# Kernel tuning notes

Measured on AMD Instinct MI355X. Metric: run time of the kernel, lower is better.

The kernel has to match this reference:

```python
import jax, jax.numpy as jnp
import numpy as np

B, N, P, E = 64, 512, 256, 4096          # batch, nodes (stations), partition nodes, edges
NUM_NWP, LP, F = 8, 16, 32               # num_nwp, local_points, local_cnn_dims
NT, ED, H, W = 8, 8, 64, 8               # num_temp, edge_feature_dims, decf_mlp_hidden, weight_function_dim
G, RH = 64, 256                          # gnn_dim, readout_hid_dim
H1, Q = 128, 9                           # mlp_hid_dim1, num quantiles


def setup_inputs() -> dict:
    key = jax.random.key(0)
    ks = iter(jax.random.split(key, 40))
    def rn(shape, s=0.05):
        return jax.random.normal(next(ks), shape, dtype=jnp.float32) * s
    # one-hot incidence matrices: each edge has one left (partition) node and one right node
    lidx = jax.random.randint(next(ks), (E,), 0, P)
    ridx = jax.random.randint(next(ks), (E,), 0, N)
    linc = jnp.zeros((P, E), jnp.float32).at[lidx, jnp.arange(E)].set(1.0)
    rinc = jnp.zeros((E, N), jnp.float32).at[jnp.arange(E), ridx].set(1.0)
    inp = {
        "x1": jax.random.normal(next(ks), (B, NUM_NWP * N, LP), dtype=jnp.float32),
        "x2": jax.random.normal(next(ks), (B, NT), dtype=jnp.float32),
        # LocalConv1D grouped conv (torch OIW layout: [Cout, Cin/groups, K])
        "conv_w": rn((F * N, NUM_NWP, LP)), "conv_b": rn((F * N,)),
        # WDSGCN2 edge-weight MLP
        "k1_w": rn((H, ED)), "k1_b": rn((H,)),
        "k2_w": rn((H, NT)),
        "k3_w": rn((H, F)),
        "k4_w": rn((H, F)),
        "k5_w": rn((W, H)), "k5_b": rn((W,)),
        "gc_w": rn((G, F * W)), "gc_b": rn((G,)),
        # readout
        "r0_w": rn((RH, G * P)),
        "r1_w": rn((RH, NT)), "r1_b": rn((RH,)),
        "r2_w": rn((RH, P)),
        "r3_w": rn((P, RH)), "r3_b": rn((P,)),
        # SMlp (forward uses l1 -> ELU -> l3 only)
        "l1_w": rn((H1, NT + G)), "l1_b": rn((H1,)),
        "l3_w": rn((Q, H1)), "l3_b": rn((Q,)),
        # buffers
        "ef": jax.random.normal(next(ks), (E, ED + 1), dtype=jnp.float32),
        "linc": linc,
        "rinc": rinc,
        "cap_feature": jax.random.normal(next(ks), (P,), dtype=jnp.float32),
        "partition_idx": jnp.arange(P, dtype=jnp.int32) * (N // P),
    }
    return inp


def reference(x1, x2, conv_w, conv_b, k1_w, k1_b, k2_w, k3_w, k4_w, k5_w, k5_b,
              gc_w, gc_b, r0_w, r1_w, r1_b, r2_w, r3_w, r3_b,
              l1_w, l1_b, l3_w, l3_b, ef, linc, rinc, cap_feature, partition_idx):
    b = x1.shape[0]
    # --- LocalConv1D: grouped conv1d (valid padding, output length 1) + ReLU ---
    y = jax.lax.conv_general_dilated(x1, conv_w, (1,), 'VALID',
                                     dimension_numbers=('NCH', 'OIH', 'NCH'),
                                     feature_group_count=N)
    x = jax.nn.relu(y + conv_b[None, :, None]).reshape(b, N, F)      # [B,N,F]
    # --- WDSGCN2: per-edge weight kernel ---
    kern = ef[:, :-1] @ k1_w.T + k1_b                                # [E,H]
    kern = kern[None] + (x2 @ k2_w.T)[:, None, :]                    # [B,E,H]
    xp = x[:, partition_idx, :]                                      # [B,P,F]
    kern = kern + jnp.einsum('pe,bpf->bef', linc, xp) @ k3_w.T       # left-node feats
    rx = jnp.einsum('en,bnf->bef', rinc, x)                          # right-node feats [B,E,F]
    kern = kern + rx @ k4_w.T
    kern = jax.nn.relu(jax.nn.leaky_relu(kern, 0.02) @ k5_w.T + k5_b)  # [B,E,W]
    # --- message = kernel (outer) right-node features, aggregated by left incidence ---
    msg = kern[:, :, :, None] * rx[:, :, None, :]                    # [B,E,W,F]
    agg = jnp.einsum('pe,bewf->bpwf', linc, msg).reshape(b, P, W * F)
    yg = jax.nn.relu(agg @ gc_w.T + gc_b)                            # [B,P,G]
    # --- readout attention over partition nodes ---
    h = yg.reshape(b, -1) @ r0_w.T + (x2 @ r1_w.T + r1_b) + cap_feature @ r2_w.T
    wt = jax.nn.relu(jax.nn.leaky_relu(h, 0.01) @ r3_w.T + r3_b)     # [B,P]
    res = jnp.einsum('bp,bpg->bg', wt, yg)                           # [B,G]
    # --- SMlp head ---
    z = jnp.concatenate([res, x2], axis=1)
    z = jax.nn.elu(z @ l1_w.T + l1_b)
    return z @ l3_w.T + l3_b                                         # [B,Q]
```

## Files before the change

### kernel.cpp

```cpp
#include <hip/hip_runtime.h>
#include <math.h>

#define B_ 64
#define N_ 512
#define P_ 256
#define E_ 4096
#define F_ 32
#define H_ 64
#define W_ 8
#define G_ 64
#define RH_ 256

#define X_OFF   0
#define T4_OFF  (X_OFF + N_*B_*F_)
#define T3_OFF  (T4_OFF + N_*B_*H_)
#define KB_OFF  (T3_OFF + P_*B_*H_)
#define KW_OFF  (KB_OFF + E_*H_)
#define YG_OFF  (KW_OFF + E_*B_*W_)
#define HB_OFF  (YG_OFF + B_*P_*G_)
#define RES_OFF (HB_OFF + B_*RH_)
#define INT_OFF (RES_OFF + 4*B_*G_)

__global__ __launch_bounds__(256) void k_decode(const float* __restrict__ linc,
    const float* __restrict__ rinc, int* __restrict__ lidx, int* __restrict__ ridx) {
  int i4 = blockIdx.x * 256 + threadIdx.x;
  const int L4 = (P_ * E_) / 4;
  if (i4 < L4) {
    float4 v = ((const float4*)linc)[i4];
    int i = i4 * 4;
    int p = i >> 12, e = i & 4095;
    if (v.x != 0.0f) lidx[e]     = p;
    if (v.y != 0.0f) lidx[e + 1] = p;
    if (v.z != 0.0f) lidx[e + 2] = p;
    if (v.w != 0.0f) lidx[e + 3] = p;
  } else {
    int j4 = i4 - L4;
    float4 v = ((const float4*)rinc)[j4];
    int j = j4 * 4;
    int e = j >> 9, n = j & 511;
    if (v.x != 0.0f) ridx[e] = n;
    if (v.y != 0.0f) ridx[e] = n + 1;
    if (v.z != 0.0f) ridx[e] = n + 2;
    if (v.w != 0.0f) ridx[e] = n + 3;
  }
}

__global__ __launch_bounds__(1024) void k_lists(const int* __restrict__ lidx,
    int* __restrict__ part_start, int* __restrict__ part_edges) {
  __shared__ int cnt[256];
  __shared__ int buf[256];
  __shared__ int cur[256];
  int t = threadIdx.x;
  if (t < 256) cnt[t] = 0;
  __syncthreads();
  for (int e = t; e < E_; e += 1024) atomicAdd(&cnt[lidx[e]], 1);
  __syncthreads();
  if (t < 256) buf[t] = cnt[t];
  __syncthreads();
  for (int off = 1; off < 256; off <<= 1) {
    int add = 0;
    if (t < 256 && t >= off) add = buf[t - off];
    __syncthreads();
    if (t < 256) buf[t] += add;
    __syncthreads();
  }
  if (t < 256) {
    part_start[t + 1] = buf[t];
    if (t == 0) part_start[0] = 0;
    cur[t] = buf[t] - cnt[t];
  }
  __syncthreads();
  for (int e = t; e < E_; e += 1024) {
    int p = lidx[e];
    int pos = atomicAdd(&cur[p], 1);
    part_edges[pos] = e;
  }
}

__global__ __launch_bounds__(256) void k_conv(const float* __restrict__ x1,
    const float* __restrict__ conv_w, const float* __restrict__ conv_b,
    float* __restrict__ x) {
  __shared__ float wsm[32 * 132];
  __shared__ float xsm[8192];
  int n = blockIdx.x, t = threadIdx.x;
  for (int i = t; i < 1024; i += 256) {
    int f = i >> 5, j = i & 31;
    ((float4*)wsm)[f * 33 + j] = ((const float4*)(conv_w + n * 4096))[i];
  }
  for (int i = t; i < 2048; i += 256) {
    int b = i >> 5, j = i & 31;
    ((float4*)xsm)[i] = ((const float4*)(x1 + b * 65536 + n * 128))[j];
  }
  __syncthreads();
  int f = t & 31, bq = t >> 5;
  float cb = conv_b[n * 32 + f];
  float acc[8];
#pragma unroll
  for (int bi = 0; bi < 8; bi++) acc[bi] = cb;
  const float4* wf4 = (const float4*)wsm + f * 33;
  const float4* xb4 = (const float4*)xsm + bq * 256;
#pragma unroll 4
  for (int k4 = 0; k4 < 32; k4++) {
    float4 wv = wf4[k4];
#pragma unroll
    for (int bi = 0; bi < 8; bi++) {
      float4 xv = xb4[bi * 32 + k4];
      acc[bi] += wv.x * xv.x + wv.y * xv.y + wv.z * xv.z + wv.w * xv.w;
    }
  }
#pragma unroll
  for (int bi = 0; bi < 8; bi++) {
    int b = bq * 8 + bi;
    x[n * 2048 + b * 32 + f] = fmaxf(acc[bi], 0.0f);
  }
}

__global__ __launch_bounds__(256) void k_prep(
    const float* __restrict__ x, const int* __restrict__ pidx,
    const float* __restrict__ k3_w, const float* __restrict__ k4_w,
    const float* __restrict__ x2, const float* __restrict__ k2_w,
    const float* __restrict__ ef, const float* __restrict__ k1_w,
    const float* __restrict__ k1_b,
    const float* __restrict__ r1_w, const float* __restrict__ r1_b,
    const float* __restrict__ r2_w, const float* __restrict__ cap,
    float* __restrict__ t4, float* __restrict__ t3, float* __restrict__ kb,
    float* __restrict__ hbuf) {
  __shared__ float xsh[2048];
  __shared__ float wsh[64 * 36];
  __shared__ float x2s[512];
  __shared__ float k2s[512];
  int blk = blockIdx.x, t = threadIdx.x;
  if (blk < 768) {
    bool isT4 = blk < 512;
    int n = isT4 ? blk : pidx[blk - 512];
    const float* wmat = isT4 ? k4_w : k3_w;
    float* outp = isT4 ? (t4 + blk * 4096) : (t3 + (blk - 512) * 4096);
    for (int i = t; i < 512; i += 256) {
      ((float4*)xsh)[i] = ((const float4*)(x + n * 2048))[i];
      int h = i >> 3, j = i & 7;
      ((float4*)wsh)[h * 9 + j] = ((const float4*)wmat)[i];
    }
    if (isT4) {
      for (int i = t; i < 128; i += 256) {
        ((float4*)x2s)[i] = ((const float4*)x2)[i];
        ((float4*)k2s)[i] = ((const float4*)k2_w)[i];
      }
    }
    __syncthreads();
    int h = t & 63, bq = t >> 6;
    float wreg[32];
#pragma unroll
    for (int j = 0; j < 8; j++) {
      float4 v = ((float4*)wsh)[h * 9 + j];
      wreg[4 * j] = v.x; wreg[4 * j + 1] = v.y; wreg[4 * j + 2] = v.z; wreg[4 * j + 3] = v.w;
    }
    float w2[8];
    if (isT4) {
      float4 u = ((float4*)k2s)[h * 2], v = ((float4*)k2s)[h * 2 + 1];
      w2[0] = u.x; w2[1] = u.y; w2[2] = u.z; w2[3] = u.w;
      w2[4] = v.x; w2[5] = v.y; w2[6] = v.z; w2[7] = v.w;
    }
    for (int bi = 0; bi < 16; bi++) {
      int b = bq * 16 + bi;
      float acc = 0.0f;
#pragma unroll
      for (int j = 0; j < 8; j++) {
        float4 xv = ((float4*)xsh)[b * 8 + j];
        acc += xv.x * wreg[4 * j] + xv.y * wreg[4 * j + 1] +
               xv.z * wreg[4 * j + 2] + xv.w * wreg[4 * j + 3];
      }
      if (isT4) {
        float4 u = ((float4*)x2s)[b * 2], v = ((float4*)x2s)[b * 2 + 1];
        acc += u.x * w2[0] + u.y * w2[1] + u.z * w2[2] + u.w * w2[3] +
               v.x * w2[4] + v.y * w2[5] + v.z * w2[6] + v.w * w2[7];
      }
      outp[b * 64 + h] = acc;
    }
  } else if (blk < 1792) {
    int o = (blk - 768) * 256 + t;
    int e = o >> 6, h = o & 63;
    float acc = k1_b[h];
    const float* er = ef + e * 9;
    const float* kr = k1_w + h * 8;
#pragma unroll
    for (int d = 0; d < 8; d++) acc += er[d] * kr[d];
    kb[o] = acc;
  } else {
    int o = (blk - 1792) * 256 + t;
    int rh = o & 255;
    float acc = r1_b[rh];
    const float* xr = x2 + (o >> 8) * 8;
    const float* rr = r1_w + rh * 8;
#pragma unroll
    for (int d = 0; d < 8; d++) acc += xr[d] * rr[d];
    const float* r2r = r2_w + rh * 256;
    for (int p4 = 0; p4 < 64; p4++) {
      float4 cv = ((const float4*)cap)[p4];
      float4 rv = ((const float4*)r2r)[p4];
      acc += cv.x * rv.x + cv.y * rv.y + cv.z * rv.z + cv.w * rv.w;
    }
    hbuf[o] = acc;
  }
}

__global__ __launch_bounds__(256) void k_edge(
    const float* __restrict__ kb, const float* __restrict__ t3,
    const float* __restrict__ t4, const float* __restrict__ k5_w,
    const float* __restrict__ k5_b, const int* __restrict__ lidx,
    const int* __restrict__ ridx, float* __restrict__ kw) {
  __shared__ float k5t[4 * 520];
  int e0 = blockIdx.x * 4, t = threadIdx.x;
  for (int i = t; i < 512; i += 256) {
    int h = i >> 3, w = i & 7;
    float v = k5_w[w * 64 + h];
#pragma unroll
    for (int qq = 0; qq < 4; qq++) k5t[qq * 520 + i] = v;
  }
  int q = t & 3, b = t >> 2;
  const float* kq = k5t + q * 520 + q * 128;
  float kb5_0 = k5_b[2 * q], kb5_1 = k5_b[2 * q + 1];
  __syncthreads();
  for (int ei = 0; ei < 4; ei++) {
    int e = e0 + ei;
    int p = lidx[e], r = ridx[e];
    const float4* kb4 = (const float4*)(kb + e * 64 + q * 16);
    const float4* t34 = (const float4*)(t3 + p * 4096 + b * 64 + q * 16);
    const float4* t44 = (const float4*)(t4 + r * 4096 + b * 64 + q * 16);
    float lk[16];
#pragma unroll
    for (int j4 = 0; j4 < 4; j4++) {
      float4 a = kb4[j4], c = t34[j4], d = t44[j4];
      float v;
      v = a.x + c.x + d.x; lk[j4 * 4 + 0] = v > 0.0f ? v : 0.02f * v;
      v = a.y + c.y + d.y; lk[j4 * 4 + 1] = v > 0.0f ? v : 0.02f * v;
      v = a.z + c.z + d.z; lk[j4 * 4 + 2] = v > 0.0f ? v : 0.02f * v;
      v = a.w + c.w + d.w; lk[j4 * 4 + 3] = v > 0.0f ? v : 0.02f * v;
    }
    float pw[8] = {0, 0, 0, 0, 0, 0, 0, 0};
#pragma unroll
    for (int j = 0; j < 16; j++) {
      float4 u = *(const float4*)(kq + j * 8);
      float4 v = *(const float4*)(kq + j * 8 + 4);
      float l = lk[j];
      pw[0] += l * u.x; pw[1] += l * u.y; pw[2] += l * u.z; pw[3] += l * u.w;
      pw[4] += l * v.x; pw[5] += l * v.y; pw[6] += l * v.z; pw[7] += l * v.w;
    }
#pragma unroll
    for (int w = 0; w < 8; w++) {
      pw[w] += __shfl_xor(pw[w], 1);
      pw[w] += __shfl_xor(pw[w], 2);
    }
    float2 o;
    o.x = fmaxf(pw[2 * q] + kb5_0, 0.0f);
    o.y = fmaxf(pw[2 * q + 1] + kb5_1, 0.0f);
    *(float2*)(kw + e * 512 + t * 2) = o;
  }
}

__global__ __launch_bounds__(256) void k_agg_gc(const float* __restrict__ x,
    const float* __restrict__ kw, const int* __restrict__ ridx,
    const int* __restrict__ part_start, const int* __restrict__ part_edges,
    const float* __restrict__ gc_w, const float* __restrict__ gc_b,
    float* __restrict__ yg) {
  __shared__ unsigned short accS[64 * 256];
  int p = blockIdx.x, t = threadIdx.x;
  int b = t >> 2, s = t & 3;
  float acc[64];
#pragma unroll
  for (int j = 0; j < 64; j++) acc[j] = 0.0f;
  int s0 = part_start[p], s1 = part_start[p + 1];
  int idx = s0;
  for (; idx + 1 < s1; idx += 2) {
    int e0 = part_edges[idx], e1 = part_edges[idx + 1];
    int r0 = ridx[e0], r1 = ridx[e1];
    float2 ka = *(const float2*)(kw + e0 * 512 + b * 8 + s * 2);
    float2 kc = *(const float2*)(kw + e1 * 512 + b * 8 + s * 2);
    const float4* xp0 = (const float4*)(x + r0 * 2048 + b * 32);
    const float4* xp1 = (const float4*)(x + r1 * 2048 + b * 32);
    float xa[32], xb[32];
#pragma unroll
    for (int i = 0; i < 8; i++) {
      float4 v = xp0[i];
      xa[4 * i] = v.x; xa[4 * i + 1] = v.y; xa[4 * i + 2] = v.z; xa[4 * i + 3] = v.w;
    }
#pragma unroll
    for (int i = 0; i < 8; i++) {
      float4 v = xp1[i];
      xb[4 * i] = v.x; xb[4 * i + 1] = v.y; xb[4 * i + 2] = v.z; xb[4 * i + 3] = v.w;
    }
#pragma unroll
    for (int j = 0; j < 32; j++) acc[j] += ka.x * xa[j];
#pragma unroll
    for (int j = 0; j < 32; j++) acc[32 + j] += ka.y * xa[j];
#pragma unroll
    for (int j = 0; j < 32; j++) acc[j] += kc.x * xb[j];
#pragma unroll
    for (int j = 0; j < 32; j++) acc[32 + j] += kc.y * xb[j];
  }
  if (idx < s1) {
    int e0 = part_edges[idx];
    int r0 = ridx[e0];
    float2 ka = *(const float2*)(kw + e0 * 512 + b * 8 + s * 2);
    const float4* xp0 = (const float4*)(x + r0 * 2048 + b * 32);
    float xa[32];
#pragma unroll
    for (int i = 0; i < 8; i++) {
      float4 v = xp0[i];
      xa[4 * i] = v.x; xa[4 * i + 1] = v.y; xa[4 * i + 2] = v.z; xa[4 * i + 3] = v.w;
    }
#pragma unroll
    for (int j = 0; j < 32; j++) acc[j] += ka.x * xa[j];
#pragma unroll
    for (int j = 0; j < 32; j++) acc[32 + j] += ka.y * xa[j];
  }
#pragma unroll
  for (int o = 0; o < 8; o++) {
    int koct = s * 8 + o;
    int os = koct ^ (b >> 3);
    unsigned int wds[4];
#pragma unroll
    for (int h = 0; h < 4; h++) {
      unsigned int u0 = __float_as_uint(acc[o * 8 + 2 * h]);
      u0 = u0 + 0x7fffu + ((u0 >> 16) & 1u);
      unsigned int u1 = __float_as_uint(acc[o * 8 + 2 * h + 1]);
      u1 = u1 + 0x7fffu + ((u1 >> 16) & 1u);
      wds[h] = (u0 >> 16) | (u1 & 0xffff0000u);
    }
    int4 pk = make_int4((int)wds[0], (int)wds[1], (int)wds[2], (int)wds[3]);
    *(int4*)(accS + b * 256 + os * 8) = pk;
  }
  __syncthreads();
  int lane = t & 63, wv = t >> 6;
  int bg = lane >> 3, gg = lane & 7;
  int g0 = wv * 16 + gg * 2;
  const float* gw0 = gc_w + g0 * 256;
  const float* gw1 = gc_w + (g0 + 1) * 256;
  float ac[8][2];
#pragma unroll
  for (int i = 0; i < 8; i++) { ac[i][0] = 0.0f; ac[i][1] = 0.0f; }
  for (int oct = 0; oct < 32; oct++) {
    int4 a8[8];
#pragma unroll
    for (int i = 0; i < 8; i++) {
      int row = bg * 8 + i;
      int os = oct ^ bg;
      a8[i] = *(const int4*)(accS + row * 256 + os * 8);
    }
    float4 b0a = *(const float4*)(gw0 + oct * 8);
    float4 b0b = *(const float4*)(gw0 + oct * 8 + 4);
    float4 b1a = *(const float4*)(gw1 + oct * 8);
    float4 b1b = *(const float4*)(gw1 + oct * 8 + 4);
    float bv0[8] = {b0a.x, b0a.y, b0a.z, b0a.w, b0b.x, b0b.y, b0b.z, b0b.w};
    float bv1[8] = {b1a.x, b1a.y, b1a.z, b1a.w, b1b.x, b1b.y, b1b.z, b1b.w};
#pragma unroll
    for (int kk = 0; kk < 8; kk++) {
#pragma unroll
      for (int i = 0; i < 8; i++) {
        int w32;
        switch (kk >> 1) {
          case 0: w32 = a8[i].x; break;
          case 1: w32 = a8[i].y; break;
          case 2: w32 = a8[i].z; break;
          default: w32 = a8[i].w; break;
        }
        unsigned int u = (unsigned int)w32;
        unsigned int bits = (kk & 1) ? (u & 0xffff0000u) : (u << 16);
        float av = __uint_as_float(bits);
        ac[i][0] += av * bv0[kk];
        ac[i][1] += av * bv1[kk];
      }
    }
  }
  float gb0 = gc_b[g0], gb1 = gc_b[g0 + 1];
#pragma unroll
  for (int i = 0; i < 8; i++) {
    int bb = bg * 8 + i;
    float* yp = yg + bb * 16384 + p * 64;
    yp[g0]     = fmaxf(ac[i][0] + gb0, 0.0f);
    yp[g0 + 1] = fmaxf(ac[i][1] + gb1, 0.0f);
  }
}

__global__ __launch_bounds__(256) void k_r0(const float* __restrict__ yg,
    const float* __restrict__ r0_w, float* __restrict__ part) {
  __shared__ float ygs[64 * 68];
  __shared__ float wts[64 * 260];
  int kc = blockIdx.x, t = threadIdx.x;
  int k0 = kc * 64;
  {
    int rr = t >> 4, c = t & 15;
    for (int rd = 0; rd < 16; rd++) {
      int rh = rd * 16 + rr;
      float4 v = *(const float4*)(r0_w + rh * 16384 + k0 + c * 4);
      wts[(4 * c + 0) * 260 + rh] = v.x;
      wts[(4 * c + 1) * 260 + rh] = v.y;
      wts[(4 * c + 2) * 260 + rh] = v.z;
      wts[(4 * c + 3) * 260 + rh] = v.w;
    }
  }
  {
    int b = t >> 2, kq = t & 3;
    const float* src = yg + b * 16384 + k0 + kq * 16;
#pragma unroll
    for (int u = 0; u < 4; u++) {
      float4 v = *(const float4*)(src + u * 4);
      int kk = kq * 16 + u * 4;
      ygs[(kk + 0) * 68 + b] = v.x;
      ygs[(kk + 1) * 68 + b] = v.y;
      ygs[(kk + 2) * 68 + b] = v.z;
      ygs[(kk + 3) * 68 + b] = v.w;
    }
  }
  __syncthreads();
  int lane = t & 63, wv = t >> 6;
  int b8 = lane & 7, r8 = lane >> 3;
  const float* yp = ygs + b8 * 8;
  const float* wp = wts + wv * 64 + r8 * 8;
  float acc[8][8];
#pragma unroll
  for (int i = 0; i < 8; i++)
#pragma unroll
    for (int j = 0; j < 8; j++) acc[i][j] = 0.0f;
#pragma unroll 2
  for (int k = 0; k < 64; k++) {
    float4 ya = *(const float4*)(yp + k * 68);
    float4 yb = *(const float4*)(yp + k * 68 + 4);
    float4 wa = *(const float4*)(wp + k * 260);
    float4 wb = *(const float4*)(wp + k * 260 + 4);
    float yv[8] = {ya.x, ya.y, ya.z, ya.w, yb.x, yb.y, yb.z, yb.w};
    float wr[8] = {wa.x, wa.y, wa.z, wa.w, wb.x, wb.y, wb.z, wb.w};
#pragma unroll
    for (int i = 0; i < 8; i++)
#pragma unroll
      for (int j = 0; j < 8; j++) acc[i][j] += yv[i] * wr[j];
  }
  float* pb = part + kc * 16384 + wv * 64 + r8 * 8;
#pragma unroll
  for (int i = 0; i < 8; i++) {
    float4 s0 = make_float4(acc[i][0], acc[i][1], acc[i][2], acc[i][3]);
    float4 s1 = make_float4(acc[i][4], acc[i][5], acc[i][6], acc[i][7]);
    float* pp = pb + (b8 * 8 + i) * 256;
    *(float4*)pp = s0;
    *(float4*)(pp + 4) = s1;
  }
}

__global__ __launch_bounds__(256) void k_r0red(const float* __restrict__ part,
    float* __restrict__ hbuf) {
  int blk = blockIdx.x;
  int oq = blk & 63, kq = blk >> 6;
  int o = oq * 256 + threadIdx.x;
  float s = 0.0f;
  const float* pp = part + kq * 64 * 16384 + o;
#pragma unroll 8
  for (int kc = 0; kc < 64; kc++) s += pp[kc * 16384];
  atomicAdd(&hbuf[o], s);
}

__global__ __launch_bounds__(256) void k_wt_res(const float* __restrict__ hbuf,
    const float* __restrict__ r3_w, const float* __restrict__ r3_b,
    const float* __restrict__ yg, float* __restrict__ res4) {
  __shared__ float hs[256];
  __shared__ float wts[64];
  __shared__ float red[256];
  int blk = blockIdx.x;
  int bb = blk >> 2, pq = blk & 3;
  int t = threadIdx.x;
  float hv = hbuf[bb * 256 + t];
  hs[t] = hv > 0.0f ? hv : 0.01f * hv;
  __syncthreads();
  int pl = t >> 2, c = t & 3;
  int pp = pq * 64 + pl;
  const float4* wrow = (const float4*)(r3_w + pp * 256 + c * 64);
  const float4* h4 = (const float4*)(hs) + c * 16;
  float a = 0.0f;
#pragma unroll
  for (int j = 0; j < 16; j++) {
    float4 w4 = wrow[j], hh = h4[j];
    a += hh.x * w4.x + hh.y * w4.y + hh.z * w4.z + hh.w * w4.w;
  }
  a += __shfl_xor(a, 1);
  a += __shfl_xor(a, 2);
  if (c == 0) wts[pl] = fmaxf(a + r3_b[pp], 0.0f);
  __syncthreads();
  int g = t & 63, ch = t >> 6;
  float r = 0.0f;
  const float* ygp = yg + bb * 16384 + pq * 4096 + g;
#pragma unroll
  for (int pi = 0; pi < 16; pi++) {
    int pl2 = ch * 16 + pi;
    r += wts[pl2] * ygp[pl2 * 64];
  }
  red[t] = r;
  __syncthreads();
  if (t < 64)
    res4[pq * 4096 + bb * 64 + t] = red[t] + red[t + 64] + red[t + 128] + red[t + 192];
}

__global__ __launch_bounds__(128) void k_final(const float* __restrict__ res4,
    const float* __restrict__ x2, const float* __restrict__ l1_w,
    const float* __restrict__ l1_b, const float* __restrict__ l3_w,
    const float* __restrict__ l3_b, float* __restrict__ out) {
  __shared__ float zs[128];
  int bb = blockIdx.x, t = threadIdx.x;
  float acc = l1_b[t];
  const float* wrow = l1_w + t * 72;
  const float* rr = res4 + bb * 64;
#pragma unroll 8
  for (int j = 0; j < 64; j++) {
    float rv = rr[j] + rr[4096 + j] + rr[8192 + j] + rr[12288 + j];
    acc += rv * wrow[j];
  }
  const float* xr = x2 + bb * 8;
#pragma unroll
  for (int j = 0; j < 8; j++) acc += xr[j] * wrow[64 + j];
  zs[t] = acc > 0.0f ? acc : expm1f(acc);
  __syncthreads();
  if (t < 9) {
    float o = l3_b[t];
    const float* w3 = l3_w + t * 128;
    for (int j = 0; j < 128; j++) o += zs[j] * w3[j];
    out[bb * 9 + t] = o;
  }
}

extern "C" void kernel_launch(void* const* d_in, const int* in_sizes, int n_in,
                              void* d_out, int out_size, void* d_ws, size_t ws_size,
                              hipStream_t stream) {
  (void)in_sizes; (void)n_in; (void)out_size; (void)ws_size;
  const float* x1     = (const float*)d_in[0];
  const float* x2     = (const float*)d_in[1];
  const float* conv_w = (const float*)d_in[2];
  const float* conv_b = (const float*)d_in[3];
  const float* k1_w   = (const float*)d_in[4];
  const float* k1_b   = (const float*)d_in[5];
  const float* k2_w   = (const float*)d_in[6];
  const float* k3_w   = (const float*)d_in[7];
  const float* k4_w   = (const float*)d_in[8];
  const float* k5_w   = (const float*)d_in[9];
  const float* k5_b   = (const float*)d_in[10];
  const float* gc_w   = (const float*)d_in[11];
  const float* gc_b   = (const float*)d_in[12];
  const float* r0_w   = (const float*)d_in[13];
  const float* r1_w   = (const float*)d_in[14];
  const float* r1_b   = (const float*)d_in[15];
  const float* r2_w   = (const float*)d_in[16];
  const float* r3_w   = (const float*)d_in[17];
  const float* r3_b   = (const float*)d_in[18];
  const float* l1_w   = (const float*)d_in[19];
  const float* l1_b   = (const float*)d_in[20];
  const float* l3_w   = (const float*)d_in[21];
  const float* l3_b   = (const float*)d_in[22];
  const float* ef     = (const float*)d_in[23];
  const float* linc   = (const float*)d_in[24];
  const float* rinc   = (const float*)d_in[25];
  const float* cap    = (const float*)d_in[26];
  const int*   pidx   = (const int*)d_in[27];
  float* out = (float*)d_out;

  float* ws   = (float*)d_ws;
  float* xbuf = ws + X_OFF;
  float* t4   = ws + T4_OFF;
  float* t3   = ws + T3_OFF;
  float* kb   = ws + KB_OFF;
  float* kwb  = ws + KW_OFF;
  float* yg   = ws + YG_OFF;
  float* hbuf = ws + HB_OFF;
  float* res4 = ws + RES_OFF;
  float* part = ws + X_OFF;
  int* ib = (int*)(ws + INT_OFF);
  int* lidx = ib;
  int* ridx = ib + 4096;
  int* part_start = ib + 8192;
  int* part_edges = ib + 8704;

  hipLaunchKernelGGL(k_decode, dim3(3072), dim3(256), 0, stream, linc, rinc, lidx, ridx);
  hipLaunchKernelGGL(k_lists, dim3(1), dim3(1024), 0, stream, lidx, part_start, part_edges);
  hipLaunchKernelGGL(k_conv, dim3(512), dim3(256), 0, stream, x1, conv_w, conv_b, xbuf);
  hipLaunchKernelGGL(k_prep, dim3(1856), dim3(256), 0, stream,
                     xbuf, pidx, k3_w, k4_w, x2, k2_w, ef, k1_w, k1_b,
                     r1_w, r1_b, r2_w, cap, t4, t3, kb, hbuf);
  hipLaunchKernelGGL(k_edge, dim3(1024), dim3(256), 0, stream,
                     kb, t3, t4, k5_w, k5_b, lidx, ridx, kwb);
  hipLaunchKernelGGL(k_agg_gc, dim3(256), dim3(256), 0, stream,
                     xbuf, kwb, ridx, part_start, part_edges, gc_w, gc_b, yg);
  hipLaunchKernelGGL(k_r0, dim3(256), dim3(256), 0, stream, yg, r0_w, part);
  hipLaunchKernelGGL(k_r0red, dim3(256), dim3(256), 0, stream, part, hbuf);
  hipLaunchKernelGGL(k_wt_res, dim3(256), dim3(256), 0, stream, hbuf, r3_w, r3_b, yg, res4);
  hipLaunchKernelGGL(k_final, dim3(64), dim3(128), 0, stream,
                     res4, x2, l1_w, l1_b, l3_w, l3_b, out);
}
```

Measured before the change: 264.4 us.

## Fuse edge-weight MLP into per-partition aggregation kernel, drop kw buffer

Merges the per-edge kernel-weight computation into the per-partition aggregation and graph-conv kernel. Each block now stages its partition's t3 rows in shared memory and computes edge weights on the fly while accumulating messages. It also prefetches the next edge index. This removes the 8 MB kw intermediate write and reread and one launch. In exchange the aggregation loop does more work per edge, serialised per partition, over only 256 blocks. It also swaps the thread index mapping in the r0 weight transpose load.

```diff
diff --git a/kernel.cpp b/kernel.cpp
--- a/kernel.cpp
+++ b/kernel.cpp
@@ -203,33 +203,51 @@
   }
 }
 
-__global__ __launch_bounds__(256) void k_edge(
-    const float* __restrict__ kb, const float* __restrict__ t3,
-    const float* __restrict__ t4, const float* __restrict__ k5_w,
-    const float* __restrict__ k5_b, const int* __restrict__ lidx,
-    const int* __restrict__ ridx, float* __restrict__ kw) {
+__global__ __launch_bounds__(256) void k_eagg(
+    const float* __restrict__ x, const float* __restrict__ kb,
+    const float* __restrict__ t3, const float* __restrict__ t4,
+    const float* __restrict__ k5_w, const float* __restrict__ k5_b,
+    const int* __restrict__ ridx, const int* __restrict__ part_start,
+    const int* __restrict__ part_edges,
+    const float* __restrict__ gc_w, const float* __restrict__ gc_b,
+    float* __restrict__ yg) {
+  __shared__ float t3s[64 * 68];
   __shared__ float k5t[4 * 520];
-  int e0 = blockIdx.x * 4, t = threadIdx.x;
+  __shared__ unsigned short accS[64 * 256];
+  int p = blockIdx.x, t = threadIdx.x;
   for (int i = t; i < 512; i += 256) {
     int h = i >> 3, w = i & 7;
     float v = k5_w[w * 64 + h];
 #pragma unroll
     for (int qq = 0; qq < 4; qq++) k5t[qq * 520 + i] = v;
   }
-  int q = t & 3, b = t >> 2;
-  const float* kq = k5t + q * 520 + q * 128;
-  float kb5_0 = k5_b[2 * q], kb5_1 = k5_b[2 * q + 1];
-  __syncthreads();
-  for (int ei = 0; ei < 4; ei++) {
-    int e = e0 + ei;
-    int p = lidx[e], r = ridx[e];
-    const float4* kb4 = (const float4*)(kb + e * 64 + q * 16);
-    const float4* t34 = (const float4*)(t3 + p * 4096 + b * 64 + q * 16);
-    const float4* t44 = (const float4*)(t4 + r * 4096 + b * 64 + q * 16);
+  for (int i4 = t; i4 < 1024; i4 += 256) {
+    float4 v = ((const float4*)(t3 + p * 4096))[i4];
+    *(float4*)(t3s + (i4 >> 4) * 68 + (i4 & 15) * 4) = v;
+  }
+  __syncthreads();
+  int s = t & 3, b = t >> 2;
+  const float* kq = k5t + s * 520 + s * 128;
+  float kb5_0 = k5_b[2 * s], kb5_1 = k5_b[2 * s + 1];
+  const float4* t3p = (const float4*)(t3s + b * 68 + s * 16);
+  float acc[64];
+#pragma unroll
+  for (int j = 0; j < 64; j++) acc[j] = 0.0f;
+  int s0 = part_start[p], s1 = part_start[p + 1];
+  int e = 0, r = 0;
+  if (s0 < s1) { e = part_edges[s0]; r = ridx[e]; }
+  for (int idx = s0; idx < s1; idx++) {
+    int e_n = 0, r_n = 0;
+    if (idx + 1 < s1) { e_n = part_edges[idx + 1]; r_n = ridx[e_n]; }
+    const float4* xp = (const float4*)(x + r * 2048 + b * 32);
+    float4 xv0 = xp[0], xv1 = xp[1], xv2 = xp[2], xv3 = xp[3];
+    float4 xv4 = xp[4], xv5 = xp[5], xv6 = xp[6], xv7 = xp[7];
+    const float4* kb4 = (const float4*)(kb + e * 64 + s * 16);
+    const float4* t44 = (const float4*)(t4 + r * 4096 + b * 64 + s * 16);
     float lk[16];
 #pragma unroll
     for (int j4 = 0; j4 < 4; j4++) {
-      float4 a = kb4[j4], c = t34[j4], d = t44[j4];
+      float4 a = kb4[j4], c = t3p[j4], d = t44[j4];
       float v;
       v = a.x + c.x + d.x; lk[j4 * 4 + 0] = v > 0.0f ? v : 0.02f * v;
       v = a.y + c.y + d.y; lk[j4 * 4 + 1] = v > 0.0f ? v : 0.02f * v;
@@ -250,68 +268,22 @@
       pw[w] += __shfl_xor(pw[w], 1);
       pw[w] += __shfl_xor(pw[w], 2);
     }
-    float2 o;
-    o.x = fmaxf(pw[2 * q] + kb5_0, 0.0f);
-    o.y = fmaxf(pw[2 * q + 1] + kb5_1, 0.0f);
-    *(float2*)(kw + e * 512 + t * 2) = o;
-  }
-}
-
-__global__ __launch_bounds__(256) void k_agg_gc(const float* __restrict__ x,
-    const float* __restrict__ kw, const int* __restrict__ ridx,
-    const int* __restrict__ part_start, const int* __restrict__ part_edges,
-    const float* __restrict__ gc_w, const float* __restrict__ gc_b,
-    float* __restrict__ yg) {
-  __shared__ unsigned short accS[64 * 256];
-  int p = blockIdx.x, t = threadIdx.x;
-  int b = t >> 2, s = t & 3;
-  float acc[64];
-#pragma unroll
-  for (int j = 0; j < 64; j++) acc[j] = 0.0f;
-  int s0 = part_start[p], s1 = part_start[p + 1];
-  int idx = s0;
-  for (; idx + 1 < s1; idx += 2) {
-    int e0 = part_edges[idx], e1 = part_edges[idx + 1];
-    int r0 = ridx[e0], r1 = ridx[e1];
-    float2 ka = *(const float2*)(kw + e0 * 512 + b * 8 + s * 2);
-    float2 kc = *(const float2*)(kw + e1 * 512 + b * 8 + s * 2);
-    const float4* xp0 = (const float4*)(x + r0 * 2048 + b * 32);
-    const float4* xp1 = (const float4*)(x + r1 * 2048 + b * 32);
-    float xa[32], xb[32];
-#pragma unroll
-    for (int i = 0; i < 8; i++) {
-      float4 v = xp0[i];
-      xa[4 * i] = v.x; xa[4 * i + 1] = v.y; xa[4 * i + 2] = v.z; xa[4 * i + 3] = v.w;
-    }
-#pragma unroll
-    for (int i = 0; i < 8; i++) {
-      float4 v = xp1[i];
-      xb[4 * i] = v.x; xb[4 * i + 1] = v.y; xb[4 * i + 2] = v.z; xb[4 * i + 3] = v.w;
-    }
-#pragma unroll
-    for (int j = 0; j < 32; j++) acc[j] += ka.x * xa[j];
-#pragma unroll
-    for (int j = 0; j < 32; j++) acc[32 + j] += ka.y * xa[j];
-#pragma unroll
-    for (int j = 0; j < 32; j++) acc[j] += kc.x * xb[j];
-#pragma unroll
-    for (int j = 0; j < 32; j++) acc[32 + j] += kc.y * xb[j];
-  }
-  if (idx < s1) {
-    int e0 = part_edges[idx];
-    int r0 = ridx[e0];
-    float2 ka = *(const float2*)(kw + e0 * 512 + b * 8 + s * 2);
-    const float4* xp0 = (const float4*)(x + r0 * 2048 + b * 32);
+    float kv0 = fmaxf(pw[2 * s] + kb5_0, 0.0f);
+    float kv1 = fmaxf(pw[2 * s + 1] + kb5_1, 0.0f);
     float xa[32];
-#pragma unroll
-    for (int i = 0; i < 8; i++) {
-      float4 v = xp0[i];
-      xa[4 * i] = v.x; xa[4 * i + 1] = v.y; xa[4 * i + 2] = v.z; xa[4 * i + 3] = v.w;
-    }
-#pragma unroll
-    for (int j = 0; j < 32; j++) acc[j] += ka.x * xa[j];
-#pragma unroll
-    for (int j = 0; j < 32; j++) acc[32 + j] += ka.y * xa[j];
+    xa[0] = xv0.x; xa[1] = xv0.y; xa[2] = xv0.z; xa[3] = xv0.w;
+    xa[4] = xv1.x; xa[5] = xv1.y; xa[6] = xv1.z; xa[7] = xv1.w;
+    xa[8] = xv2.x; xa[9] = xv2.y; xa[10] = xv2.z; xa[11] = xv2.w;
+    xa[12] = xv3.x; xa[13] = xv3.y; xa[14] = xv3.z; xa[15] = xv3.w;
+    xa[16] = xv4.x; xa[17] = xv4.y; xa[18] = xv4.z; xa[19] = xv4.w;
+    xa[20] = xv5.x; xa[21] = xv5.y; xa[22] = xv5.z; xa[23] = xv5.w;
+    xa[24] = xv6.x; xa[25] = xv6.y; xa[26] = xv6.z; xa[27] = xv6.w;
+    xa[28] = xv7.x; xa[29] = xv7.y; xa[30] = xv7.z; xa[31] = xv7.w;
+#pragma unroll
+    for (int j = 0; j < 32; j++) acc[j] += kv0 * xa[j];
+#pragma unroll
+    for (int j = 0; j < 32; j++) acc[32 + j] += kv1 * xa[j];
+    e = e_n; r = r_n;
   }
 #pragma unroll
   for (int o = 0; o < 8; o++) {
@@ -388,7 +360,7 @@
   int kc = blockIdx.x, t = threadIdx.x;
   int k0 = kc * 64;
   {
-    int rr = t >> 4, c = t & 15;
+    int c = t >> 4, rr = t & 15;
     for (int rd = 0; rd < 16; rd++) {
       int rh = rd * 16 + rr;
       float4 v = *(const float4*)(r0_w + rh * 16384 + k0 + c * 4);
@@ -563,7 +535,6 @@
   float* t4   = ws + T4_OFF;
   float* t3   = ws + T3_OFF;
   float* kb   = ws + KB_OFF;
-  float* kwb  = ws + KW_OFF;
   float* yg   = ws + YG_OFF;
   float* hbuf = ws + HB_OFF;
   float* res4 = ws + RES_OFF;
@@ -580,10 +551,9 @@
   hipLaunchKernelGGL(k_prep, dim3(1856), dim3(256), 0, stream,
                      xbuf, pidx, k3_w, k4_w, x2, k2_w, ef, k1_w, k1_b,
                      r1_w, r1_b, r2_w, cap, t4, t3, kb, hbuf);
-  hipLaunchKernelGGL(k_edge, dim3(1024), dim3(256), 0, stream,
-                     kb, t3, t4, k5_w, k5_b, lidx, ridx, kwb);
-  hipLaunchKernelGGL(k_agg_gc, dim3(256), dim3(256), 0, stream,
-                     xbuf, kwb, ridx, part_start, part_edges, gc_w, gc_b, yg);
+  hipLaunchKernelGGL(k_eagg, dim3(256), dim3(256), 0, stream,
+                     xbuf, kb, t3, t4, k5_w, k5_b, ridx, part_start, part_edges,
+                     gc_w, gc_b, yg);
   hipLaunchKernelGGL(k_r0, dim3(256), dim3(256), 0, stream, yg, r0_w, part);
   hipLaunchKernelGGL(k_r0red, dim3(256), dim3(256), 0, stream, part, hbuf);
   hipLaunchKernelGGL(k_wt_res, dim3(256), dim3(256), 0, stream, hbuf, r3_w, r3_b, yg, res4);
```

Result: faster. 259.0 us (-2.0%).
